# Performance work log

Hardware: AMD Instinct MI355X
Metric: run time of the kernel (lower is better)

Reference implementation:

```python
import jax, jax.numpy as jnp
import numpy as np

B, R, K_RANK = 128, 256, 10  # batch, rDim==cDim, rank
MU = 0.1
GAMMA = 0.51 * MU


def averaging_diagonals(X):
    """Project [..., m, n] matrices to Toeplitz by averaging each diagonal."""
    m, n = X.shape[-2:]
    # diagonal id for entry (i, j): j - i + (m - 1), in [0, m + n - 2]
    idx = (jnp.arange(n)[None, :] - jnp.arange(m)[:, None] + (m - 1)).reshape(-1)
    D = m + n - 1
    lead = X.shape[:-2]
    flat = X.reshape(lead + (m * n,))
    sums = jnp.zeros(lead + (D,), X.dtype).at[..., idx].add(flat)
    counts = jnp.zeros((D,), X.dtype).at[idx].add(jnp.ones((m * n,), X.dtype))
    avg = sums / counts
    return avg[..., idx].reshape(X.shape)


def rank_k(x, K):
    """Best rank-K approximation via truncated SVD, batched over leading dims."""
    U, S, Vh = jnp.linalg.svd(x, full_matrices=False)
    return jnp.einsum('...rk,...k,...kc->...rc', U[..., :K], S[..., :K], Vh[..., :K, :])


def setup_inputs() -> dict:
    key = jax.random.key(0)
    k1, k2, k3 = jax.random.split(key, 3)
    T = jax.random.normal(k1, (B, R, R), jnp.float32)
    Tp = jax.random.normal(k2, (B, R, R), jnp.float32)
    Sp = jax.random.normal(k3, (B, R, R), jnp.float32)
    # generateW: averagingDiagonals of indicator of first row/col
    S0 = jnp.zeros((R, R), jnp.float32).at[0, :].set(1.0).at[:, 0].set(1.0)
    W = averaging_diagonals(S0)
    w1 = jnp.eye(R, dtype=jnp.float32) * (1.0 - GAMMA)
    w2 = jnp.eye(R, dtype=jnp.float32) * GAMMA
    w3 = MU * W
    w4 = -MU * W
    return {"T": T, "Tp": Tp, "Sp": Sp, "w1": w1, "w2": w2, "w3": w3, "w4": w4, "K": K_RANK}


def reference(T, Tp, Sp, w1, w2, w3, w4, K):
    # Tptmp = w1 @ Sp + w2 @ Tp + w4 * Tp + w3 * T  (batched over B)
    Tptmp = (jnp.einsum('rk,bkc->brc', w1, Sp)
             + jnp.einsum('rk,bkc->brc', w2, Tp)
             + w4 * Tp + w3 * T)
    Tpnew = rank_k(Tptmp, K)
    Spnew = Sp - Tpnew + averaging_diagonals(2.0 * Tpnew - Sp)
    return (T, Tpnew, Spnew)
```

## Files before the change

kernel.cpp:

```cpp
#include <hip/hip_runtime.h>
#include <math.h>

#define B_   128
#define N_   256
#define L_   64
#define NRR  (N_*N_)
#define BRR  (B_*NRR)
#define BNL  (B_*N_*L_)

static __device__ __forceinline__ void fma4(float4& a, float s, const float4& v) {
  a.x += s * v.x; a.y += s * v.y; a.z += s * v.z; a.w += s * v.w;
}

__global__ __launch_bounds__(256) void k_build_A(
    const float* __restrict__ T, const float* __restrict__ Tp,
    const float* __restrict__ Sp, const float* __restrict__ w1,
    const float* __restrict__ w2, const float* __restrict__ w3,
    const float* __restrict__ w4, float* __restrict__ A) {
  int i4 = blockIdx.x * 256 + threadIdx.x;
  if (i4 >= BRR / 4) return;
  int rc4 = i4 & (NRR / 4 - 1);
  int r = rc4 >> 6;
  float a1 = w1[r * N_ + r], a2 = w2[r * N_ + r];
  float4 sp = ((const float4*)Sp)[i4];
  float4 tp = ((const float4*)Tp)[i4];
  float4 tt = ((const float4*)T)[i4];
  float4 w3v = ((const float4*)w3)[rc4];
  float4 w4v = ((const float4*)w4)[rc4];
  float4 o;
  o.x = a1 * sp.x + a2 * tp.x + w4v.x * tp.x + w3v.x * tt.x;
  o.y = a1 * sp.y + a2 * tp.y + w4v.y * tp.y + w3v.y * tt.y;
  o.z = a1 * sp.z + a2 * tp.z + w4v.z * tp.z + w3v.z * tt.z;
  o.w = a1 * sp.w + a2 * tp.w + w4v.w * tp.w + w3v.w * tt.w;
  ((float4*)A)[i4] = o;
}

__global__ __launch_bounds__(256) void k_aat(const float* __restrict__ A,
                                             float* __restrict__ G) {
  int b = blockIdx.z, ti = blockIdx.x, tj = blockIdx.y;
  if (ti > tj) return;
  int it = ti * 64, jt = tj * 64;
  __shared__ __align__(16) float AsT[32][68];
  __shared__ __align__(16) float BsT[32][68];
  const float* Ab = A + (size_t)b * NRR;
  int t = threadIdx.x, tx = t & 15, ty = t >> 4;
  float4 acc[4] = {};
  int kk = t & 31, r0 = t >> 5;
  for (int k0 = 0; k0 < N_; k0 += 32) {
#pragma unroll
    for (int p = 0; p < 8; ++p) {
      int r = r0 + p * 8;
      AsT[kk][r] = Ab[(it + r) * N_ + k0 + kk];
      BsT[kk][r] = Ab[(jt + r) * N_ + k0 + kk];
    }
    __syncthreads();
#pragma unroll
    for (int k = 0; k < 32; ++k) {
      float4 av = *(const float4*)&AsT[k][ty * 4];
      float4 bv = *(const float4*)&BsT[k][tx * 4];
      fma4(acc[0], av.x, bv);
      fma4(acc[1], av.y, bv);
      fma4(acc[2], av.z, bv);
      fma4(acc[3], av.w, bv);
    }
    __syncthreads();
  }
  float* Gb = G + (size_t)b * NRR;
#pragma unroll
  for (int i = 0; i < 4; ++i)
    *(float4*)&Gb[(it + ty * 4 + i) * N_ + jt + tx * 4] = acc[i];
  if (ti < tj) {
    const float* a = (const float*)acc;
#pragma unroll
    for (int i = 0; i < 4; ++i)
#pragma unroll
      for (int j = 0; j < 4; ++j)
        Gb[(jt + tx * 4 + j) * N_ + it + ty * 4 + i] = a[i * 4 + j];
  }
}

__global__ __launch_bounds__(256) void k_gq(const float* __restrict__ G,
                                            const float* __restrict__ Q,
                                            float* __restrict__ Y) {
  __shared__ __align__(16) float Qs[64][68];
  int b = blockIdx.y, it = blockIdx.x * 64;
  const float* Gb = G + (size_t)b * NRR;
  const float* Qb = Q + (size_t)b * (N_ * L_);
  int t = threadIdx.x, cx = t & 15, ry = t >> 4;
  const float* gr[4];
#pragma unroll
  for (int i = 0; i < 4; ++i) gr[i] = Gb + (size_t)(it + ry * 4 + i) * N_;
  float4 acc[4] = {};
  for (int kc = 0; kc < N_; kc += 64) {
#pragma unroll
    for (int p = 0; p < 4; ++p) {
      int idx = t + p * 256;
      int r = idx >> 4, c4 = idx & 15;
      *(float4*)&Qs[r][c4 * 4] = *(const float4*)&Qb[(kc + r) * L_ + c4 * 4];
    }
    __syncthreads();
#pragma unroll 4
    for (int k4 = 0; k4 < 16; ++k4) {
      int k = k4 * 4;
      float4 g[4];
#pragma unroll
      for (int i = 0; i < 4; ++i) g[i] = *(const float4*)&gr[i][kc + k];
      float4 q0 = *(const float4*)&Qs[k + 0][cx * 4];
      float4 q1 = *(const float4*)&Qs[k + 1][cx * 4];
      float4 q2 = *(const float4*)&Qs[k + 2][cx * 4];
      float4 q3 = *(const float4*)&Qs[k + 3][cx * 4];
#pragma unroll
      for (int i = 0; i < 4; ++i) {
        fma4(acc[i], g[i].x, q0);
        fma4(acc[i], g[i].y, q1);
        fma4(acc[i], g[i].z, q2);
        fma4(acc[i], g[i].w, q3);
      }
    }
    __syncthreads();
  }
  float* Yb = Y + (size_t)b * (N_ * L_);
#pragma unroll
  for (int i = 0; i < 4; ++i)
    *(float4*)&Yb[(it + ry * 4 + i) * L_ + cx * 4] = acc[i];
}

__global__ __launch_bounds__(256) void k_xty(const float* __restrict__ X,
                                             const float* __restrict__ Y,
                                             float* __restrict__ Mo) {
  int b = blockIdx.x, t = threadIdx.x, tx = t & 15, ty = t >> 4;
  const float* Xb = X + (size_t)b * (N_ * L_);
  const float* Yb = Y + (size_t)b * (N_ * L_);
  float4 a0 = {}, a1 = {}, a2 = {}, a3 = {};
#pragma unroll 4
  for (int k = 0; k < N_; ++k) {
    float4 xv = *(const float4*)&Xb[k * L_ + ty * 4];
    float4 yv = *(const float4*)&Yb[k * L_ + tx * 4];
    fma4(a0, xv.x, yv); fma4(a1, xv.y, yv);
    fma4(a2, xv.z, yv); fma4(a3, xv.w, yv);
  }
  float* Mb = Mo + (size_t)b * L_ * L_;
  *(float4*)&Mb[(ty * 4 + 0) * L_ + tx * 4] = a0;
  *(float4*)&Mb[(ty * 4 + 1) * L_ + tx * 4] = a1;
  *(float4*)&Mb[(ty * 4 + 2) * L_ + tx * 4] = a2;
  *(float4*)&Mb[(ty * 4 + 3) * L_ + tx * 4] = a3;
}

__global__ __launch_bounds__(256) void k_init_Y(float* __restrict__ Y) {
  int idx = blockIdx.x * 256 + threadIdx.x;
  if (idx >= BNL) return;
  unsigned u = (unsigned)idx * 2654435761u;
  u ^= u >> 16; u *= 2246822519u; u ^= u >> 13; u *= 3266489917u; u ^= u >> 16;
  Y[idx] = (float)(int)u * 4.6566129e-10f;
}

__global__ __launch_bounds__(256) void k_qr(float* __restrict__ Q) {
  __shared__ __align__(16) float S[64][68];
  __shared__ float dinv[64];
  int b = blockIdx.x, t = threadIdx.x, tx = t & 15, ty = t >> 4;
  float* Qb = Q + (size_t)b * (N_ * L_);
  {
    float4 a0 = {}, a1 = {}, a2 = {}, a3 = {};
#pragma unroll 4
    for (int k = 0; k < N_; ++k) {
      float4 xv = *(const float4*)&Qb[k * L_ + ty * 4];
      float4 yv = *(const float4*)&Qb[k * L_ + tx * 4];
      fma4(a0, xv.x, yv); fma4(a1, xv.y, yv);
      fma4(a2, xv.z, yv); fma4(a3, xv.w, yv);
    }
    *(float4*)&S[ty * 4 + 0][tx * 4] = a0;
    *(float4*)&S[ty * 4 + 1][tx * 4] = a1;
    *(float4*)&S[ty * 4 + 2][tx * 4] = a2;
    *(float4*)&S[ty * 4 + 3][tx * 4] = a3;
  }
  __syncthreads();
  for (int kb = 0; kb < 8; ++kb) {
    int base = kb * 8;
    if (t == 0) {
      for (int q = 0; q < 8; ++q) {
        float d = S[base + q][base + q];
        for (int w = 0; w < q; ++w) d -= S[base + q][base + w] * S[base + q][base + w];
        d = sqrtf(fmaxf(d, 1e-20f));
        S[base + q][base + q] = d;
        float di = 1.f / d;
        dinv[base + q] = di;
        for (int r = q + 1; r < 8; ++r) {
          float v = S[base + r][base + q];
          for (int w = 0; w < q; ++w) v -= S[base + r][base + w] * S[base + q][base + w];
          S[base + r][base + q] = v * di;
        }
      }
    }
    __syncthreads();
    int nrows = 56 - base;
    if (t < nrows) {
      int i = base + 8 + t;
      float x[8];
#pragma unroll
      for (int q = 0; q < 8; ++q) {
        float v = S[i][base + q];
        for (int w = 0; w < q; ++w) v -= S[base + q][base + w] * x[w];
        x[q] = v * dinv[base + q];
      }
#pragma unroll
      for (int q = 0; q < 8; ++q) S[i][base + q] = x[q];
    }
    __syncthreads();
    if (nrows > 0) {
      for (int e = t; e < nrows * 64; e += 256) {
        int io = e >> 6, ko = e & 63;
        if (ko < nrows) {
          int i = base + 8 + io, k = base + 8 + ko;
          float4 p0 = *(const float4*)&S[i][base], p1 = *(const float4*)&S[i][base + 4];
          float4 r0 = *(const float4*)&S[k][base], r1 = *(const float4*)&S[k][base + 4];
          S[i][k] -= p0.x * r0.x + p0.y * r0.y + p0.z * r0.z + p0.w * r0.w
                   + p1.x * r1.x + p1.y * r1.y + p1.z * r1.z + p1.w * r1.w;
        }
      }
    }
    __syncthreads();
  }
  {
    float x[64];
#pragma unroll
    for (int u = 0; u < 16; ++u) {
      float4 v = *(const float4*)&Qb[t * L_ + u * 4];
      x[u * 4 + 0] = v.x; x[u * 4 + 1] = v.y;
      x[u * 4 + 2] = v.z; x[u * 4 + 3] = v.w;
    }
#pragma unroll
    for (int j = 0; j < 64; ++j) {
      float s = x[j];
#pragma unroll
      for (int mq = 0; mq < (j >> 2); ++mq) {
        float4 lv = *(const float4*)&S[j][mq * 4];
        s -= lv.x * x[mq * 4 + 0] + lv.y * x[mq * 4 + 1]
           + lv.z * x[mq * 4 + 2] + lv.w * x[mq * 4 + 3];
      }
#pragma unroll
      for (int k = (j & ~3); k < j; ++k) s -= S[j][k] * x[k];
      x[j] = s * dinv[j];
    }
#pragma unroll
    for (int u = 0; u < 16; ++u) {
      float4 v;
      v.x = x[u * 4 + 0]; v.y = x[u * 4 + 1];
      v.z = x[u * 4 + 2]; v.w = x[u * 4 + 3];
      *(float4*)&Qb[t * L_ + u * 4] = v;
    }
  }
}

__global__ __launch_bounds__(256) void k_jacobi(float* __restrict__ Mg,
                                                float* __restrict__ Vg) {
  __shared__ __align__(16) float A[64][68];
  __shared__ float shist[252 * 32];
  __shared__ int selb[16];
  int b = blockIdx.x, t = threadIdx.x;
  float* Mb = Mg + (size_t)b * L_ * L_;
#pragma unroll
  for (int p = 0; p < 16; ++p) {
    int e = t + p * 256, r = e >> 6, c = e & 63;
    A[r][c] = Mb[r * L_ + c];
  }
  __syncthreads();
  int m = t >> 3, u = t & 7;
  int rcnt = 0;
  for (int sweep = 0; sweep < 4; ++sweep) {
    for (int rnd = 0; rnd < 63; ++rnd, ++rcnt) {
      int i, j;
      if (m == 0) { i = rnd; j = 63; }
      else {
        int a = rnd + m;       if (a >= 63) a -= 63;
        int bb = rnd + 63 - m; if (bb >= 63) bb -= 63;
        i = min(a, bb); j = max(a, bb);
      }
      float aii = A[i][i], ajj = A[j][j], aij = A[i][j];
      float c_ = 1.f, s_ = 0.f;
      if (fabsf(aij) > 1e-12f) {
        float tau = (ajj - aii) / (2.f * aij);
        float tt = (tau >= 0.f ? 1.f : -1.f) / (fabsf(tau) + sqrtf(1.f + tau * tau));
        c_ = rsqrtf(1.f + tt * tt);
        s_ = tt * c_;
      }
      if (u == 0) shist[rcnt * 32 + m] = s_;
      {
        float4* Ai = (float4*)&A[i][u * 8];
        float4* Aj = (float4*)&A[j][u * 8];
#pragma unroll
        for (int q = 0; q < 2; ++q) {
          float4 x = Ai[q], y = Aj[q], nx, ny;
          nx.x = c_ * x.x - s_ * y.x; ny.x = s_ * x.x + c_ * y.x;
          nx.y = c_ * x.y - s_ * y.y; ny.y = s_ * x.y + c_ * y.y;
          nx.z = c_ * x.z - s_ * y.z; ny.z = s_ * x.z + c_ * y.z;
          nx.w = c_ * x.w - s_ * y.w; ny.w = s_ * x.w + c_ * y.w;
          Ai[q] = nx; Aj[q] = ny;
        }
      }
      __syncthreads();
#pragma unroll
      for (int p = 0; p < 8; ++p) {
        int k = u + 8 * p;
        float x = A[k][i], y = A[k][j];
        A[k][i] = c_ * x - s_ * y;
        A[k][j] = s_ * x + c_ * y;
      }
      __syncthreads();
    }
  }
  int lane = t & 63, wv = t >> 6;
  float dl = A[lane][lane];
  int rank = 0;
  for (int k = 0; k < 64; ++k) {
    float dk = A[k][k];
    rank += (dk > dl || (dk == dl && k < lane)) ? 1 : 0;
  }
  if (t < 64 && rank < 16) selb[rank] = lane;
  __syncthreads();
  int s0 = selb[wv * 4 + 0], s1 = selb[wv * 4 + 1];
  int s2 = selb[wv * 4 + 2], s3 = selb[wv * 4 + 3];
  float x0 = (lane == s0) ? 1.f : 0.f;
  float x1 = (lane == s1) ? 1.f : 0.f;
  float x2 = (lane == s2) ? 1.f : 0.f;
  float x3 = (lane == s3) ? 1.f : 0.f;
  for (int rc = 251; rc >= 0; --rc) {
    int rnd = rc % 63;
    int partner, mm;
    if (lane == 63)        { partner = rnd; mm = 0; }
    else if (lane == rnd)  { partner = 63;  mm = 0; }
    else {
      partner = (2 * rnd - lane + 126) % 63;
      int mc = (lane - rnd + 63) % 63;
      mm = mc < 63 - mc ? mc : 63 - mc;
    }
    float s_ = shist[rc * 32 + mm];
    float c_ = sqrtf(fmaxf(1.f - s_ * s_, 0.f));
    float coef = (lane > partner) ? -s_ : s_;
    float y0 = __shfl(x0, partner, 64);
    float y1 = __shfl(x1, partner, 64);
    float y2 = __shfl(x2, partner, 64);
    float y3 = __shfl(x3, partner, 64);
    x0 = c_ * x0 + coef * y0;
    x1 = c_ * x1 + coef * y1;
    x2 = c_ * x2 + coef * y2;
    x3 = c_ * x3 + coef * y3;
  }
  float* Vb = Vg + (size_t)b * 1024;
  Vb[lane * 16 + wv * 4 + 0] = x0;
  Vb[lane * 16 + wv * 4 + 1] = x1;
  Vb[lane * 16 + wv * 4 + 2] = x2;
  Vb[lane * 16 + wv * 4 + 3] = x3;
}

__global__ __launch_bounds__(256) void k_formU(const float* __restrict__ Q,
                                               const float* __restrict__ Vg,
                                               const int* __restrict__ Kp,
                                               float* __restrict__ U) {
  __shared__ float Vs[64][17];
  int b = blockIdx.x, t = threadIdx.x;
  int K = *Kp; if (K > 16) K = 16;
  if (t < 64) {
    for (int j = 0; j < 16; ++j)
      Vs[t][j] = (j < K) ? Vg[(size_t)b * 1024 + t * 16 + j] : 0.f;
  }
  __syncthreads();
  const float* Qb = Q + (size_t)b * N_ * L_;
  float qv[64];
#pragma unroll
  for (int k = 0; k < 64; ++k) qv[k] = Qb[t * L_ + k];
  float* Ub = U + (size_t)b * N_ * 16;
  for (int j = 0; j < 16; ++j) {
    float s = 0.f;
    if (j < K) {
#pragma unroll
      for (int k = 0; k < 64; ++k) s += qv[k] * Vs[k][j];
    }
    Ub[t * 16 + j] = s;
  }
}

__global__ __launch_bounds__(256) void k_utA(const float* __restrict__ U,
                                             const float* __restrict__ A,
                                             const int* __restrict__ Kp,
                                             float* __restrict__ C) {
  __shared__ float Us[256][17];
  int b = blockIdx.x, t = threadIdx.x;
  int K = *Kp; if (K > 16) K = 16;
  const float* Ub = U + (size_t)b * N_ * 16;
  for (int p = 0; p < 16; ++p) {
    int r = (t >> 4) + p * 16, j = t & 15;
    Us[r][j] = Ub[r * 16 + j];
  }
  __syncthreads();
  const float* Ab = A + (size_t)b * NRR;
  float acc[16];
  for (int j = 0; j < 16; ++j) acc[j] = 0.f;
  for (int i = 0; i < N_; ++i) {
    float av = Ab[i * N_ + t];
    for (int j = 0; j < K; ++j) acc[j] += Us[i][j] * av;
  }
  float* Cb = C + (size_t)b * 16 * N_;
  for (int j = 0; j < 16; ++j) Cb[j * N_ + t] = (j < K) ? acc[j] : 0.f;
}

__global__ __launch_bounds__(256) void k_uc(const float* __restrict__ U,
                                            const float* __restrict__ C,
                                            const int* __restrict__ Kp,
                                            float* __restrict__ Tpnew) {
  __shared__ float Cs[16][256];
  __shared__ float Us[16][17];
  int b = blockIdx.y, rt = blockIdx.x * 16, t = threadIdx.x;
  int K = *Kp; if (K > 16) K = 16;
  const float* Cb = C + (size_t)b * 16 * N_;
  for (int j = 0; j < 16; ++j) Cs[j][t] = Cb[j * N_ + t];
  Us[t >> 4][t & 15] = U[(size_t)b * N_ * 16 + (size_t)(rt + (t >> 4)) * 16 + (t & 15)];
  __syncthreads();
  float* Ob = Tpnew + (size_t)b * NRR;
  for (int r = 0; r < 16; ++r) {
    float s = 0.f;
    for (int j = 0; j < K; ++j) s += Us[r][j] * Cs[j][t];
    Ob[(rt + r) * N_ + t] = s;
  }
}

__global__ __launch_bounds__(256) void k_copyT(const float* __restrict__ T,
                                               float* __restrict__ O) {
  int i4 = blockIdx.x * 256 + threadIdx.x;
  if (i4 < BRR / 4) ((float4*)O)[i4] = ((const float4*)T)[i4];
}

__global__ __launch_bounds__(256) void k_spnew(const float* __restrict__ Sp,
                                               const float* __restrict__ Tpnew,
                                               float* __restrict__ Spnew) {
  __shared__ float sums[512];
  int b = blockIdx.x, t = threadIdx.x;
  for (int i = t; i < 512; i += 256) sums[i] = 0.f;
  __syncthreads();
  const float4* Spb = (const float4*)(Sp + (size_t)b * NRR);
  const float4* Tb  = (const float4*)(Tpnew + (size_t)b * NRR);
  for (int i4 = t; i4 < NRR / 4; i4 += 256) {
    int r = i4 >> 6, c = (i4 & 63) * 4;
    float4 tv = Tb[i4], sv = Spb[i4];
    int d = c - r + 255;
    atomicAdd(&sums[d + 0], 2.f * tv.x - sv.x);
    atomicAdd(&sums[d + 1], 2.f * tv.y - sv.y);
    atomicAdd(&sums[d + 2], 2.f * tv.z - sv.z);
    atomicAdd(&sums[d + 3], 2.f * tv.w - sv.w);
  }
  __syncthreads();
  for (int d = t; d < 511; d += 256) {
    int cnt = 256 - (d < 255 ? 255 - d : d - 255);
    sums[d] /= (float)cnt;
  }
  __syncthreads();
  float4* Ob = (float4*)(Spnew + (size_t)b * NRR);
  for (int i4 = t; i4 < NRR / 4; i4 += 256) {
    int r = i4 >> 6, c = (i4 & 63) * 4;
    float4 tv = Tb[i4], sv = Spb[i4];
    int d = c - r + 255;
    float4 o;
    o.x = sv.x - tv.x + sums[d + 0];
    o.y = sv.y - tv.y + sums[d + 1];
    o.z = sv.z - tv.z + sums[d + 2];
    o.w = sv.w - tv.w + sums[d + 3];
    Ob[i4] = o;
  }
}

extern "C" void kernel_launch(void* const* d_in, const int* in_sizes, int n_in,
                              void* d_out, int out_size, void* d_ws, size_t ws_size,
                              hipStream_t stream) {
  const float* T  = (const float*)d_in[0];
  const float* Tp = (const float*)d_in[1];
  const float* Sp = (const float*)d_in[2];
  const float* w1 = (const float*)d_in[3];
  const float* w2 = (const float*)d_in[4];
  const float* w3 = (const float*)d_in[5];
  const float* w4 = (const float*)d_in[6];
  const int*   Kp = (const int*)d_in[7];
  float* out = (float*)d_out;

  float* slot0 = out;
  float* slot1 = out + BRR;
  float* slot2 = out + 2 * (size_t)BRR;
  float* G = slot0;
  float* A = slot1;
  float* Qb[2] = { slot2, slot2 + BNL };
  float* sc    = slot2 + 2 * (size_t)BNL;
  float* Mbuf  = sc;
  float* Vbuf  = sc + 524288;
  float* Ubuf  = sc + 2 * 524288;
  float* Cbuf  = sc + 3 * 524288;

  k_build_A<<<BRR / 4 / 256, 256, 0, stream>>>(T, Tp, Sp, w1, w2, w3, w4, A);
  k_aat<<<dim3(4, 4, B_), 256, 0, stream>>>(A, G);
  k_init_Y<<<BNL / 256, 256, 0, stream>>>(Qb[0]);
  k_qr<<<B_, 256, 0, stream>>>(Qb[0]);

  int cur = 0;
  for (int it = 0; it < 12; ++it) {
    k_gq<<<dim3(4, B_), 256, 0, stream>>>(G, Qb[cur], Qb[1 - cur]);
    cur = 1 - cur;
    if ((it & 3) == 3) k_qr<<<B_, 256, 0, stream>>>(Qb[cur]);
  }
  k_gq<<<dim3(4, B_), 256, 0, stream>>>(G, Qb[cur], Qb[1 - cur]);
  k_xty<<<B_, 256, 0, stream>>>(Qb[cur], Qb[1 - cur], Mbuf);
  k_jacobi<<<B_, 256, 0, stream>>>(Mbuf, Vbuf);
  k_formU<<<B_, 256, 0, stream>>>(Qb[cur], Vbuf, Kp, Ubuf);
  k_utA<<<B_, 256, 0, stream>>>(Ubuf, A, Kp, Cbuf);
  k_uc<<<dim3(16, B_), 256, 0, stream>>>(Ubuf, Cbuf, Kp, slot1);
  k_copyT<<<BRR / 4 / 256, 256, 0, stream>>>(T, slot0);
  k_spnew<<<B_, 256, 0, stream>>>(Sp, slot1, slot2);
}
```

Baseline: 1.358 ms.

## Fuse XtY, Jacobi and U formation; overlap T copy with extra blocks

Computes the small XᵀY product directly into shared memory inside the Jacobi kernel and forms U right after the eigenvector rotation, removing two launches and the global round trips for M and V. The output copy of T is moved into extra blocks of the same launch, so the memory-bound copy can overlap with the latency-bound Jacobi blocks. The cost is a heavier kernel with more shared memory and registers per block, which may lower occupancy.

```diff
diff --git a/kernel.cpp b/kernel.cpp
--- a/kernel.cpp
+++ b/kernel.cpp
@@ -125,27 +125,6 @@
     *(float4*)&Yb[(it + ry * 4 + i) * L_ + cx * 4] = acc[i];
 }
 
-__global__ __launch_bounds__(256) void k_xty(const float* __restrict__ X,
-                                             const float* __restrict__ Y,
-                                             float* __restrict__ Mo) {
-  int b = blockIdx.x, t = threadIdx.x, tx = t & 15, ty = t >> 4;
-  const float* Xb = X + (size_t)b * (N_ * L_);
-  const float* Yb = Y + (size_t)b * (N_ * L_);
-  float4 a0 = {}, a1 = {}, a2 = {}, a3 = {};
-#pragma unroll 4
-  for (int k = 0; k < N_; ++k) {
-    float4 xv = *(const float4*)&Xb[k * L_ + ty * 4];
-    float4 yv = *(const float4*)&Yb[k * L_ + tx * 4];
-    fma4(a0, xv.x, yv); fma4(a1, xv.y, yv);
-    fma4(a2, xv.z, yv); fma4(a3, xv.w, yv);
-  }
-  float* Mb = Mo + (size_t)b * L_ * L_;
-  *(float4*)&Mb[(ty * 4 + 0) * L_ + tx * 4] = a0;
-  *(float4*)&Mb[(ty * 4 + 1) * L_ + tx * 4] = a1;
-  *(float4*)&Mb[(ty * 4 + 2) * L_ + tx * 4] = a2;
-  *(float4*)&Mb[(ty * 4 + 3) * L_ + tx * 4] = a3;
-}
-
 __global__ __launch_bounds__(256) void k_init_Y(float* __restrict__ Y) {
   int idx = blockIdx.x * 256 + threadIdx.x;
   if (idx >= BNL) return;
@@ -251,17 +230,40 @@
   }
 }
 
-__global__ __launch_bounds__(256) void k_jacobi(float* __restrict__ Mg,
-                                                float* __restrict__ Vg) {
+__global__ __launch_bounds__(256) void k_jacobi(const float* __restrict__ X,
+                                                const float* __restrict__ Y,
+                                                const int* __restrict__ Kp,
+                                                float* __restrict__ U,
+                                                const float* __restrict__ Tg,
+                                                float* __restrict__ Tout) {
+  if (blockIdx.x >= 128) {
+    int tid = (blockIdx.x - 128) * 256 + threadIdx.x;
+    const float4* src = (const float4*)Tg;
+    float4* dst = (float4*)Tout;
+    for (int i = tid; i < BRR / 4; i += 128 * 256) dst[i] = src[i];
+    return;
+  }
   __shared__ __align__(16) float A[64][68];
   __shared__ float shist[252 * 32];
+  __shared__ float Vs[64][17];
   __shared__ int selb[16];
   int b = blockIdx.x, t = threadIdx.x;
-  float* Mb = Mg + (size_t)b * L_ * L_;
-#pragma unroll
-  for (int p = 0; p < 16; ++p) {
-    int e = t + p * 256, r = e >> 6, c = e & 63;
-    A[r][c] = Mb[r * L_ + c];
+  {
+    int tx = t & 15, ty = t >> 4;
+    const float* Xb = X + (size_t)b * (N_ * L_);
+    const float* Yb = Y + (size_t)b * (N_ * L_);
+    float4 a0 = {}, a1 = {}, a2 = {}, a3 = {};
+#pragma unroll 4
+    for (int k = 0; k < N_; ++k) {
+      float4 xv = *(const float4*)&Xb[k * L_ + ty * 4];
+      float4 yv = *(const float4*)&Yb[k * L_ + tx * 4];
+      fma4(a0, xv.x, yv); fma4(a1, xv.y, yv);
+      fma4(a2, xv.z, yv); fma4(a3, xv.w, yv);
+    }
+    *(float4*)&A[ty * 4 + 0][tx * 4] = a0;
+    *(float4*)&A[ty * 4 + 1][tx * 4] = a1;
+    *(float4*)&A[ty * 4 + 2][tx * 4] = a2;
+    *(float4*)&A[ty * 4 + 3][tx * 4] = a3;
   }
   __syncthreads();
   int m = t >> 3, u = t & 7;
@@ -345,37 +347,26 @@
     x2 = c_ * x2 + coef * y2;
     x3 = c_ * x3 + coef * y3;
   }
-  float* Vb = Vg + (size_t)b * 1024;
-  Vb[lane * 16 + wv * 4 + 0] = x0;
-  Vb[lane * 16 + wv * 4 + 1] = x1;
-  Vb[lane * 16 + wv * 4 + 2] = x2;
-  Vb[lane * 16 + wv * 4 + 3] = x3;
-}
-
-__global__ __launch_bounds__(256) void k_formU(const float* __restrict__ Q,
-                                               const float* __restrict__ Vg,
-                                               const int* __restrict__ Kp,
-                                               float* __restrict__ U) {
-  __shared__ float Vs[64][17];
-  int b = blockIdx.x, t = threadIdx.x;
-  int K = *Kp; if (K > 16) K = 16;
-  if (t < 64) {
-    for (int j = 0; j < 16; ++j)
-      Vs[t][j] = (j < K) ? Vg[(size_t)b * 1024 + t * 16 + j] : 0.f;
-  }
-  __syncthreads();
-  const float* Qb = Q + (size_t)b * N_ * L_;
-  float qv[64];
-#pragma unroll
-  for (int k = 0; k < 64; ++k) qv[k] = Qb[t * L_ + k];
-  float* Ub = U + (size_t)b * N_ * 16;
-  for (int j = 0; j < 16; ++j) {
-    float s = 0.f;
-    if (j < K) {
-#pragma unroll
-      for (int k = 0; k < 64; ++k) s += qv[k] * Vs[k][j];
-    }
-    Ub[t * 16 + j] = s;
+  Vs[lane][wv * 4 + 0] = x0;
+  Vs[lane][wv * 4 + 1] = x1;
+  Vs[lane][wv * 4 + 2] = x2;
+  Vs[lane][wv * 4 + 3] = x3;
+  __syncthreads();
+  {
+    int K = *Kp; if (K > 16) K = 16;
+    const float* Qb = X + (size_t)b * N_ * L_;
+    float qv[64];
+#pragma unroll
+    for (int k = 0; k < 64; ++k) qv[k] = Qb[t * L_ + k];
+    float* Ub = U + (size_t)b * N_ * 16;
+    for (int j = 0; j < 16; ++j) {
+      float s = 0.f;
+      if (j < K) {
+#pragma unroll
+        for (int k = 0; k < 64; ++k) s += qv[k] * Vs[k][j];
+      }
+      Ub[t * 16 + j] = s;
+    }
   }
 }
 
@@ -421,12 +412,6 @@
     for (int j = 0; j < K; ++j) s += Us[r][j] * Cs[j][t];
     Ob[(rt + r) * N_ + t] = s;
   }
-}
-
-__global__ __launch_bounds__(256) void k_copyT(const float* __restrict__ T,
-                                               float* __restrict__ O) {
-  int i4 = blockIdx.x * 256 + threadIdx.x;
-  if (i4 < BRR / 4) ((float4*)O)[i4] = ((const float4*)T)[i4];
 }
 
 __global__ __launch_bounds__(256) void k_spnew(const float* __restrict__ Sp,
@@ -487,8 +472,6 @@
   float* A = slot1;
   float* Qb[2] = { slot2, slot2 + BNL };
   float* sc    = slot2 + 2 * (size_t)BNL;
-  float* Mbuf  = sc;
-  float* Vbuf  = sc + 524288;
   float* Ubuf  = sc + 2 * 524288;
   float* Cbuf  = sc + 3 * 524288;
 
@@ -504,11 +487,8 @@
     if ((it & 3) == 3) k_qr<<<B_, 256, 0, stream>>>(Qb[cur]);
   }
   k_gq<<<dim3(4, B_), 256, 0, stream>>>(G, Qb[cur], Qb[1 - cur]);
-  k_xty<<<B_, 256, 0, stream>>>(Qb[cur], Qb[1 - cur], Mbuf);
-  k_jacobi<<<B_, 256, 0, stream>>>(Mbuf, Vbuf);
-  k_formU<<<B_, 256, 0, stream>>>(Qb[cur], Vbuf, Kp, Ubuf);
+  k_jacobi<<<256, 256, 0, stream>>>(Qb[cur], Qb[1 - cur], Kp, Ubuf, T, slot0);
   k_utA<<<B_, 256, 0, stream>>>(Ubuf, A, Kp, Cbuf);
   k_uc<<<dim3(16, B_), 256, 0, stream>>>(Ubuf, Cbuf, Kp, slot1);
-  k_copyT<<<BRR / 4 / 256, 256, 0, stream>>>(T, slot0);
   k_spnew<<<B_, 256, 0, stream>>>(Sp, slot1, slot2);
 }
```

Result: no change. 1.339 ms (-1.4%).
